# Performance work log

Hardware: AMD Instinct MI355X
Metric: run time of the kernel (lower is better)

## Reference

```python
import jax, jax.numpy as jnp
import numpy as np

# Fuzzy-logic decoder: rules = [[0,0,0],[1,0,1]] (hardcoded in the torch module's __init__).
# For each rule [p, a, b] firing on predicate p:
#   num[s,o] = max_k min(t[a, s, k], t[b, k, o])   (max-min relation composition)
# amalgamate(x, y) = x + y - x*y (probabilistic OR); new starts at 0, and
# amalgamate(x, 0) = x, so with exactly one rule per predicate:
#   t_new[p] = amalgamate(t[p], num_p) = t[p] + num_p - t[p]*num_p

def _compose(A, B):
    # A: [S, K], B: [K, O] -> max over k of elementwise min -> [S, O]
    return jnp.max(jnp.minimum(A[:, :, None], B[None, :, :]), axis=1)


def setup_inputs() -> dict:
    key = jax.random.key(0)
    t = jax.random.uniform(key, (2, 512, 512), dtype=jnp.float32)
    return {"t": t}


def reference(t) -> jnp.ndarray:
    t0, t1 = t[0], t[1]
    num0 = _compose(t0, t0)          # rule [0,0,0]
    num1 = _compose(t0, t1)          # rule [1,0,1]
    num = jnp.stack([num0, num1], axis=0)  # [2, S, O]
    return t + num - t * num         # amalgamate(t, num)
```

## Files before the change

### kernel.cpp

```cpp
#include <hip/hip_runtime.h>


#define SDIM 512
#define TS 32
#define TO 64
#define KHALF 256
#define BK 64
#define BK2 32
#define NCH (KHALF / BK)
#define ASTR 34
#define BSTR 68

typedef _Float16 h2 __attribute__((ext_vector_type(2)));

__device__ __forceinline__ h2 pack2(float a, float b) {
    return __builtin_bit_cast(h2, __builtin_amdgcn_cvt_pkrtz(a, b));
}
__device__ __forceinline__ h2 pmin(h2 a, h2 b) { return __builtin_elementwise_min(a, b); }
__device__ __forceinline__ h2 pmax(h2 a, h2 b) { return __builtin_elementwise_max(a, b); }
__device__ __forceinline__ h2 bch2(unsigned u) { return __builtin_bit_cast(h2, u); }
__device__ __forceinline__ unsigned bcu(h2 v) { return __builtin_bit_cast(unsigned, v); }

__global__ __launch_bounds__(256, 2) void compose_partial(
        const float* __restrict__ t, float* __restrict__ out) {
    __shared__ h2 Als[BK2][ASTR];
    __shared__ h2 Bls[BK2][BSTR];

    const int tid = threadIdx.x;
    const int o0 = blockIdx.x * TO;
    const int s0 = blockIdx.y * TS;
    const int p  = blockIdx.z >> 1;
    const int kh = blockIdx.z & 1;
    const int kb = kh * KHALF;

    const float* __restrict__ B = t + p * (SDIM * SDIM);

    const int ol = (tid & 15) * 4;
    const int sl = (tid >> 4) * 2;
    const int ar = tid >> 3, aq = tid & 7;
    const int bk2 = tid >> 3, bq = tid & 7;

    const float4* __restrict__ Arow =
        reinterpret_cast<const float4*>(t + (s0 + ar) * SDIM);

    h2 acc[2][4];
    #pragma unroll
    for (int j = 0; j < 2; ++j)
        #pragma unroll
        for (int i = 0; i < 4; ++i) acc[j][i] = pack2(0.f, 0.f);

    float4 fa0, fa1, fx, fx2, fy, fy2;
    {
        const int kf = kb / 4 + aq * 2;
        fa0 = Arow[kf];
        fa1 = Arow[kf + 1];
        const float* __restrict__ Bb = B + (kb + 2 * bk2) * SDIM + o0 + bq * 8;
        fx  = *reinterpret_cast<const float4*>(Bb);
        fx2 = *reinterpret_cast<const float4*>(Bb + 4);
        fy  = *reinterpret_cast<const float4*>(Bb + SDIM);
        fy2 = *reinterpret_cast<const float4*>(Bb + SDIM + 4);
    }

    for (int c = 0; c < NCH; ++c) {
        {
            const int k2b = aq * 4;
            Als[k2b + 0][ar] = pack2(fa0.x, fa0.y);
            Als[k2b + 1][ar] = pack2(fa0.z, fa0.w);
            Als[k2b + 2][ar] = pack2(fa1.x, fa1.y);
            Als[k2b + 3][ar] = pack2(fa1.z, fa1.w);
            uint4 u0, u1;
            u0.x = bcu(pack2(fx.x, fy.x));
            u0.y = bcu(pack2(fx.y, fy.y));
            u0.z = bcu(pack2(fx.z, fy.z));
            u0.w = bcu(pack2(fx.w, fy.w));
            u1.x = bcu(pack2(fx2.x, fy2.x));
            u1.y = bcu(pack2(fx2.y, fy2.y));
            u1.z = bcu(pack2(fx2.z, fy2.z));
            u1.w = bcu(pack2(fx2.w, fy2.w));
            *reinterpret_cast<uint4*>(&Bls[bk2][bq * 8]) = u0;
            *reinterpret_cast<uint4*>(&Bls[bk2][bq * 8 + 4]) = u1;
        }
        __syncthreads();

        if (c + 1 < NCH) {
            const int k0 = kb + (c + 1) * BK;
            const int kf = k0 / 4 + aq * 2;
            fa0 = Arow[kf];
            fa1 = Arow[kf + 1];
            const float* __restrict__ Bb = B + (k0 + 2 * bk2) * SDIM + o0 + bq * 8;
            fx  = *reinterpret_cast<const float4*>(Bb);
            fx2 = *reinterpret_cast<const float4*>(Bb + 4);
            fy  = *reinterpret_cast<const float4*>(Bb + SDIM);
            fy2 = *reinterpret_cast<const float4*>(Bb + SDIM + 4);
        }

        #pragma unroll
        for (int k2 = 0; k2 < BK2; ++k2) {
            const uint2 ua = *reinterpret_cast<const uint2*>(&Als[k2][sl]);
            const uint4 ub = *reinterpret_cast<const uint4*>(&Bls[k2][ol]);
            const h2 a0 = bch2(ua.x), a1 = bch2(ua.y);
            const h2 b0 = bch2(ub.x), b1 = bch2(ub.y);
            const h2 b2 = bch2(ub.z), b3 = bch2(ub.w);
            acc[0][0] = pmax(acc[0][0], pmin(a0, b0));
            acc[0][1] = pmax(acc[0][1], pmin(a0, b1));
            acc[0][2] = pmax(acc[0][2], pmin(a0, b2));
            acc[0][3] = pmax(acc[0][3], pmin(a0, b3));
            acc[1][0] = pmax(acc[1][0], pmin(a1, b0));
            acc[1][1] = pmax(acc[1][1], pmin(a1, b1));
            acc[1][2] = pmax(acc[1][2], pmin(a1, b2));
            acc[1][3] = pmax(acc[1][3], pmin(a1, b3));
        }
        __syncthreads();
    }

    unsigned short* __restrict__ op = reinterpret_cast<unsigned short*>(out);
    #pragma unroll
    for (int j = 0; j < 2; ++j) {
        const int row = s0 + sl + j;
        #pragma unroll
        for (int i = 0; i < 4; ++i) {
            const int o = o0 + ol + i;
            const float nm = fmaxf((float)acc[j][i][0], (float)acc[j][i][1]);
            const _Float16 hh = (_Float16)nm;
            op[(((p * SDIM) + row) * SDIM + o) * 2 + kh] =
                __builtin_bit_cast(unsigned short, hh);
        }
    }
}

__global__ __launch_bounds__(256) void combine_amalg(
        const float* __restrict__ t, float* __restrict__ out) {
    const int idx = blockIdx.x * 256 + threadIdx.x;
    const uint4 w = reinterpret_cast<const uint4*>(out)[idx];
    const float4 tv = reinterpret_cast<const float4*>(t)[idx];
    const unsigned wv[4] = {w.x, w.y, w.z, w.w};
    const float tf[4] = {tv.x, tv.y, tv.z, tv.w};
    float rs[4];
    #pragma unroll
    for (int i = 0; i < 4; ++i) {
        const _Float16 h0 = __builtin_bit_cast(_Float16, (unsigned short)(wv[i] & 0xffffu));
        const _Float16 h1 = __builtin_bit_cast(_Float16, (unsigned short)(wv[i] >> 16));
        const float num = fmaxf((float)h0, (float)h1);
        rs[i] = tf[i] + num - tf[i] * num;
    }
    float4 r;
    r.x = rs[0]; r.y = rs[1]; r.z = rs[2]; r.w = rs[3];
    reinterpret_cast<float4*>(out)[idx] = r;
}

extern "C" void kernel_launch(void* const* d_in, const int* in_sizes, int n_in,
                              void* d_out, int out_size, void* d_ws, size_t ws_size,
                              hipStream_t stream) {
    const float* t = (const float*)d_in[0];
    float* out = (float*)d_out;
    dim3 g1(SDIM / TO, SDIM / TS, 4);
    compose_partial<<<g1, 256, 0, stream>>>(t, out);
    combine_amalg<<<dim3(512), 256, 0, stream>>>(t, out);
}
```

Before: 71.43 us.

## Stage whole K-half in LDS once and vectorize partial-result layout

```diff
diff --git a/kernel.cpp b/kernel.cpp
--- a/kernel.cpp
+++ b/kernel.cpp
@@ -5,9 +5,7 @@
 #define TS 32
 #define TO 64
 #define KHALF 256
-#define BK 64
-#define BK2 32
-#define NCH (KHALF / BK)
+#define K2H 128
 #define ASTR 34
 #define BSTR 68
 
@@ -23,8 +21,8 @@
 
 __global__ __launch_bounds__(256, 2) void compose_partial(
         const float* __restrict__ t, float* __restrict__ out) {
-    __shared__ h2 Als[BK2][ASTR];
-    __shared__ h2 Bls[BK2][BSTR];
+    __shared__ h2 Als[K2H][ASTR];
+    __shared__ h2 Bls[K2H][BSTR];
 
     const int tid = threadIdx.x;
     const int o0 = blockIdx.x * TO;
@@ -33,15 +31,44 @@
     const int kh = blockIdx.z & 1;
     const int kb = kh * KHALF;
 
-    const float* __restrict__ B = t + p * (SDIM * SDIM);
+    const float* __restrict__ Bp = t + p * (SDIM * SDIM);
+
+    const int ar = tid >> 3, aq = tid & 7;
+    const float4* __restrict__ Arow =
+        reinterpret_cast<const float4*>(t + (s0 + ar) * SDIM + kb);
+    float4 fa[8];
+    #pragma unroll
+    for (int j = 0; j < 8; ++j) fa[j] = Arow[aq + 8 * j];
+
+    const int bq = tid & 15, bp = tid >> 4;
+    const float* __restrict__ Bb = Bp + kb * SDIM + o0 + bq * 4;
+    float4 fx[8], fy[8];
+    #pragma unroll
+    for (int j = 0; j < 8; ++j) {
+        const int r2 = (bp + 16 * j) * 2;
+        fx[j] = *reinterpret_cast<const float4*>(Bb + r2 * SDIM);
+        fy[j] = *reinterpret_cast<const float4*>(Bb + (r2 + 1) * SDIM);
+    }
+
+    #pragma unroll
+    for (int j = 0; j < 8; ++j) {
+        const int k2b = 2 * (aq + 8 * j);
+        Als[k2b    ][ar] = pack2(fa[j].x, fa[j].y);
+        Als[k2b + 1][ar] = pack2(fa[j].z, fa[j].w);
+    }
+    #pragma unroll
+    for (int j = 0; j < 8; ++j) {
+        uint4 u;
+        u.x = bcu(pack2(fx[j].x, fy[j].x));
+        u.y = bcu(pack2(fx[j].y, fy[j].y));
+        u.z = bcu(pack2(fx[j].z, fy[j].z));
+        u.w = bcu(pack2(fx[j].w, fy[j].w));
+        *reinterpret_cast<uint4*>(&Bls[bp + 16 * j][bq * 4]) = u;
+    }
+    __syncthreads();
 
     const int ol = (tid & 15) * 4;
     const int sl = (tid >> 4) * 2;
-    const int ar = tid >> 3, aq = tid & 7;
-    const int bk2 = tid >> 3, bq = tid & 7;
-
-    const float4* __restrict__ Arow =
-        reinterpret_cast<const float4*>(t + (s0 + ar) * SDIM);
 
     h2 acc[2][4];
     #pragma unroll
@@ -49,103 +76,54 @@
         #pragma unroll
         for (int i = 0; i < 4; ++i) acc[j][i] = pack2(0.f, 0.f);
 
-    float4 fa0, fa1, fx, fx2, fy, fy2;
-    {
-        const int kf = kb / 4 + aq * 2;
-        fa0 = Arow[kf];
-        fa1 = Arow[kf + 1];
-        const float* __restrict__ Bb = B + (kb + 2 * bk2) * SDIM + o0 + bq * 8;
-        fx  = *reinterpret_cast<const float4*>(Bb);
-        fx2 = *reinterpret_cast<const float4*>(Bb + 4);
-        fy  = *reinterpret_cast<const float4*>(Bb + SDIM);
-        fy2 = *reinterpret_cast<const float4*>(Bb + SDIM + 4);
+    #pragma unroll 8
+    for (int k2 = 0; k2 < K2H; ++k2) {
+        const uint2 ua = *reinterpret_cast<const uint2*>(&Als[k2][sl]);
+        const uint4 ub = *reinterpret_cast<const uint4*>(&Bls[k2][ol]);
+        const h2 a0 = bch2(ua.x), a1 = bch2(ua.y);
+        const h2 b0 = bch2(ub.x), b1 = bch2(ub.y);
+        const h2 b2 = bch2(ub.z), b3 = bch2(ub.w);
+        acc[0][0] = pmax(acc[0][0], pmin(a0, b0));
+        acc[0][1] = pmax(acc[0][1], pmin(a0, b1));
+        acc[0][2] = pmax(acc[0][2], pmin(a0, b2));
+        acc[0][3] = pmax(acc[0][3], pmin(a0, b3));
+        acc[1][0] = pmax(acc[1][0], pmin(a1, b0));
+        acc[1][1] = pmax(acc[1][1], pmin(a1, b1));
+        acc[1][2] = pmax(acc[1][2], pmin(a1, b2));
+        acc[1][3] = pmax(acc[1][3], pmin(a1, b3));
     }
 
-    for (int c = 0; c < NCH; ++c) {
-        {
-            const int k2b = aq * 4;
-            Als[k2b + 0][ar] = pack2(fa0.x, fa0.y);
-            Als[k2b + 1][ar] = pack2(fa0.z, fa0.w);
-            Als[k2b + 2][ar] = pack2(fa1.x, fa1.y);
-            Als[k2b + 3][ar] = pack2(fa1.z, fa1.w);
-            uint4 u0, u1;
-            u0.x = bcu(pack2(fx.x, fy.x));
-            u0.y = bcu(pack2(fx.y, fy.y));
-            u0.z = bcu(pack2(fx.z, fy.z));
-            u0.w = bcu(pack2(fx.w, fy.w));
-            u1.x = bcu(pack2(fx2.x, fy2.x));
-            u1.y = bcu(pack2(fx2.y, fy2.y));
-            u1.z = bcu(pack2(fx2.z, fy2.z));
-            u1.w = bcu(pack2(fx2.w, fy2.w));
-            *reinterpret_cast<uint4*>(&Bls[bk2][bq * 8]) = u0;
-            *reinterpret_cast<uint4*>(&Bls[bk2][bq * 8 + 4]) = u1;
-        }
-        __syncthreads();
-
-        if (c + 1 < NCH) {
-            const int k0 = kb + (c + 1) * BK;
-            const int kf = k0 / 4 + aq * 2;
-            fa0 = Arow[kf];
-            fa1 = Arow[kf + 1];
-            const float* __restrict__ Bb = B + (k0 + 2 * bk2) * SDIM + o0 + bq * 8;
-            fx  = *reinterpret_cast<const float4*>(Bb);
-            fx2 = *reinterpret_cast<const float4*>(Bb + 4);
-            fy  = *reinterpret_cast<const float4*>(Bb + SDIM);
-            fy2 = *reinterpret_cast<const float4*>(Bb + SDIM + 4);
-        }
-
-        #pragma unroll
-        for (int k2 = 0; k2 < BK2; ++k2) {
-            const uint2 ua = *reinterpret_cast<const uint2*>(&Als[k2][sl]);
-            const uint4 ub = *reinterpret_cast<const uint4*>(&Bls[k2][ol]);
-            const h2 a0 = bch2(ua.x), a1 = bch2(ua.y);
-            const h2 b0 = bch2(ub.x), b1 = bch2(ub.y);
-            const h2 b2 = bch2(ub.z), b3 = bch2(ub.w);
-            acc[0][0] = pmax(acc[0][0], pmin(a0, b0));
-            acc[0][1] = pmax(acc[0][1], pmin(a0, b1));
-            acc[0][2] = pmax(acc[0][2], pmin(a0, b2));
-            acc[0][3] = pmax(acc[0][3], pmin(a0, b3));
-            acc[1][0] = pmax(acc[1][0], pmin(a1, b0));
-            acc[1][1] = pmax(acc[1][1], pmin(a1, b1));
-            acc[1][2] = pmax(acc[1][2], pmin(a1, b2));
-            acc[1][3] = pmax(acc[1][3], pmin(a1, b3));
-        }
-        __syncthreads();
-    }
-
-    unsigned short* __restrict__ op = reinterpret_cast<unsigned short*>(out);
+    unsigned short* __restrict__ us = reinterpret_cast<unsigned short*>(out);
     #pragma unroll
     for (int j = 0; j < 2; ++j) {
         const int row = s0 + sl + j;
-        #pragma unroll
-        for (int i = 0; i < 4; ++i) {
-            const int o = o0 + ol + i;
-            const float nm = fmaxf((float)acc[j][i][0], (float)acc[j][i][1]);
-            const _Float16 hh = (_Float16)nm;
-            op[(((p * SDIM) + row) * SDIM + o) * 2 + kh] =
-                __builtin_bit_cast(unsigned short, hh);
-        }
+        const int e = ((p * SDIM) + row) * SDIM + o0 + ol;
+        const float n0 = fmaxf((float)acc[j][0][0], (float)acc[j][0][1]);
+        const float n1 = fmaxf((float)acc[j][1][0], (float)acc[j][1][1]);
+        const float n2 = fmaxf((float)acc[j][2][0], (float)acc[j][2][1]);
+        const float n3 = fmaxf((float)acc[j][3][0], (float)acc[j][3][1]);
+        uint2 w;
+        w.x = bcu(pack2(n0, n1));
+        w.y = bcu(pack2(n2, n3));
+        *reinterpret_cast<uint2*>(&us[e * 2 + kh * 4]) = w;
     }
 }
 
 __global__ __launch_bounds__(256) void combine_amalg(
         const float* __restrict__ t, float* __restrict__ out) {
-    const int idx = blockIdx.x * 256 + threadIdx.x;
-    const uint4 w = reinterpret_cast<const uint4*>(out)[idx];
-    const float4 tv = reinterpret_cast<const float4*>(t)[idx];
-    const unsigned wv[4] = {w.x, w.y, w.z, w.w};
+    const int g = blockIdx.x * 256 + threadIdx.x;
+    const uint4 w = reinterpret_cast<const uint4*>(out)[g];
+    const float4 tv = reinterpret_cast<const float4*>(t)[g];
+    const h2 n01 = pmax(bch2(w.x), bch2(w.z));
+    const h2 n23 = pmax(bch2(w.y), bch2(w.w));
+    const float n[4] = {(float)n01[0], (float)n01[1], (float)n23[0], (float)n23[1]};
     const float tf[4] = {tv.x, tv.y, tv.z, tv.w};
-    float rs[4];
-    #pragma unroll
-    for (int i = 0; i < 4; ++i) {
-        const _Float16 h0 = __builtin_bit_cast(_Float16, (unsigned short)(wv[i] & 0xffffu));
-        const _Float16 h1 = __builtin_bit_cast(_Float16, (unsigned short)(wv[i] >> 16));
-        const float num = fmaxf((float)h0, (float)h1);
-        rs[i] = tf[i] + num - tf[i] * num;
-    }
     float4 r;
-    r.x = rs[0]; r.y = rs[1]; r.z = rs[2]; r.w = rs[3];
-    reinterpret_cast<float4*>(out)[idx] = r;
+    r.x = tf[0] + n[0] - tf[0] * n[0];
+    r.y = tf[1] + n[1] - tf[1] * n[1];
+    r.z = tf[2] + n[2] - tf[2] * n[2];
+    r.w = tf[3] + n[3] - tf[3] * n[3];
+    reinterpret_cast<float4*>(out)[g] = r;
 }
 
 extern "C" void kernel_launch(void* const* d_in, const int* in_sizes, int n_in,
```

Result: faster. 69.92 us (-2.1%).
